# Kernel tuning notes

Hardware: AMD Instinct MI355X
Metric: run time of the kernel (lower is better)

## Reference

```python
import jax, jax.numpy as jnp
import numpy as np

EMBED_DIM = 1024
NUM_HEADS = 16
SCALE = (EMBED_DIM // NUM_HEADS) ** -0.5  # 0.125


def setup_inputs() -> dict:
    key = jax.random.key(0)
    ks = jax.random.split(key, 9)
    B, S, E = 4, 2048, EMBED_DIM
    std = E ** -0.5
    x = jax.random.normal(ks[0], (B, S, E), dtype=jnp.float32)
    Wq = jax.random.normal(ks[1], (E, E), dtype=jnp.float32) * std
    bq = jax.random.normal(ks[2], (E,), dtype=jnp.float32) * 0.01
    Wk = jax.random.normal(ks[3], (E, E), dtype=jnp.float32) * std
    bk = jax.random.normal(ks[4], (E,), dtype=jnp.float32) * 0.01
    Wv = jax.random.normal(ks[5], (E, E), dtype=jnp.float32) * std
    bv = jax.random.normal(ks[6], (E,), dtype=jnp.float32) * 0.01
    Wo = jax.random.normal(ks[7], (E, E), dtype=jnp.float32) * std
    bo = jax.random.normal(ks[8], (E,), dtype=jnp.float32) * 0.01
    return {"x": x, "Wq": Wq, "bq": bq, "Wk": Wk, "bk": bk,
            "Wv": Wv, "bv": bv, "Wo": Wo, "bo": bo}


def reference(x, Wq, bq, Wk, bk, Wv, bv, Wo, bo):
    # torch nn.Linear: y = x @ W.T + b
    q = jnp.einsum('bse,fe->bsf', x, Wq) + bq   # [B,S,E]
    k = jnp.einsum('bse,fe->bsf', x, Wk) + bk
    v = jnp.einsum('bse,fe->bsf', x, Wv) + bv
    # Bilinear (no softmax) attention: scores = (Q K^T) * scale
    scores = jnp.einsum('bse,bte->bst', q, k) * SCALE  # [B,S,S]
    out = jnp.einsum('bst,bte->bse', scores, v)        # [B,S,E]
    return jnp.einsum('bse,fe->bsf', out, Wo) + bo
```

## Files before the change

kernel.cpp:

```cpp
#include <hip/hip_runtime.h>
#include <stdint.h>

typedef __bf16 bf16_t;
typedef __bf16 bf16x8 __attribute__((ext_vector_type(8)));
typedef __bf16 bf16x4 __attribute__((ext_vector_type(4)));
typedef float floatx4 __attribute__((ext_vector_type(4)));

__device__ __forceinline__ void async_copy16(const bf16_t* g, bf16_t* l) {
  __builtin_amdgcn_global_load_lds(
      (const __attribute__((address_space(1))) void*)g,
      (__attribute__((address_space(3))) void*)l, 16, 0, 0);
}

struct CvtSeg { const float* s; bf16_t* d; long n; };
struct CvtArgs { CvtSeg seg[5]; };

__global__ void cvt_multi(CvtArgs a) {
  CvtSeg sg = a.seg[blockIdx.y];
  long i = ((long)blockIdx.x * blockDim.x + threadIdx.x) * 4;
  if (i < sg.n) {
    float4 f = *(const float4*)(sg.s + i);
    bf16x4 o;
    o[0] = (bf16_t)f.x; o[1] = (bf16_t)f.y; o[2] = (bf16_t)f.z; o[3] = (bf16_t)f.w;
    *(bf16x4*)(sg.d + i) = o;
  }
}

__global__ void reduce2_cvt(const float* __restrict__ a, const float* __restrict__ b,
                            bf16_t* __restrict__ d, long n) {
  long i = ((long)blockIdx.x * blockDim.x + threadIdx.x) * 4;
  if (i < n) {
    float4 x = *(const float4*)(a + i);
    float4 y = *(const float4*)(b + i);
    bf16x4 o;
    o[0] = (bf16_t)(x.x + y.x); o[1] = (bf16_t)(x.y + y.y);
    o[2] = (bf16_t)(x.z + y.z); o[3] = (bf16_t)(x.w + y.w);
    *(bf16x4*)(d + i) = o;
  }
}

__device__ __forceinline__ void gemm_core(
    const bf16_t* __restrict__ Ab, const bf16_t* __restrict__ Bb,
    int lda, int ldb, int nk, bf16_t* As, bf16_t* Bs,
    int m0, int n0, floatx4 (&acc)[4][4]) {
  const int tid  = threadIdx.x;
  const int lane = tid & 63;
  const int w    = tid >> 6;
  const int wr   = w >> 1, wc = w & 1;
  const int quad = lane >> 4, lm = lane & 15;
  const int ar = lane >> 2;
  const int ak = (((lane & 3) ^ ((ar >> 1) & 3))) * 8;
  const bf16_t* ag0 = Ab + (long)(m0 + w * 16 + ar) * lda + ak;
  const bf16_t* ag1 = ag0 + (long)64 * lda;
  const bf16_t* bg0 = Bb + (long)(n0 + w * 16 + ar) * ldb + ak;
  const bf16_t* bg1 = bg0 + (long)64 * ldb;
  const int swz = (lm >> 1) & 3;

  {
    bf16_t* la = As + w * 512;
    bf16_t* lb = Bs + w * 512;
    async_copy16(ag0, la);
    async_copy16(ag1, la + 2048);
    async_copy16(bg0, lb);
    async_copy16(bg1, lb + 2048);
  }
  for (int i = 0; i < nk; i++) {
    __syncthreads();
    if (i + 1 < nk) {
      const int buf = (i + 1) & 1;
      const int k0  = (i + 1) * 32;
      bf16_t* la = As + buf * 4096 + w * 512;
      bf16_t* lb = Bs + buf * 4096 + w * 512;
      async_copy16(ag0 + k0, la);
      async_copy16(ag1 + k0, la + 2048);
      async_copy16(bg0 + k0, lb);
      async_copy16(bg1 + k0, lb + 2048);
    }
    const bf16_t* Ar = As + (i & 1) * 4096;
    const bf16_t* Br = Bs + (i & 1) * 4096;
    bf16x8 afr[4], bfr[4];
#pragma unroll
    for (int r = 0; r < 4; r++)
      afr[r] = *(const bf16x8*)&Ar[(wr * 64 + r * 16 + lm) * 32 + (quad ^ swz) * 8];
#pragma unroll
    for (int c = 0; c < 4; c++)
      bfr[c] = *(const bf16x8*)&Br[(wc * 64 + c * 16 + lm) * 32 + (quad ^ swz) * 8];
#pragma unroll
    for (int r = 0; r < 4; r++)
#pragma unroll
      for (int c = 0; c < 4; c++)
        acc[r][c] = __builtin_amdgcn_mfma_f32_16x16x32_bf16(afr[r], bfr[c], acc[r][c], 0, 0, 0);
  }
}

__global__ __launch_bounds__(256, 2) void qkv3(
    const bf16_t* __restrict__ xb,
    const bf16_t* __restrict__ Wq, const bf16_t* __restrict__ Wk, const bf16_t* __restrict__ Wv,
    const float* __restrict__ bq, const float* __restrict__ bk, const float* __restrict__ bv,
    bf16_t* __restrict__ qout, bf16_t* __restrict__ kT, bf16_t* __restrict__ vT) {
  __shared__ bf16_t As[2 * 4096];
  __shared__ bf16_t Bsh[3][2 * 4096];
  const int L = blockIdx.x + (blockIdx.y << 3) + (blockIdx.z << 7);
  const int V = (L & 7) * 64 + (L >> 3);
  const int batch = V >> 7;
  const int rr_   = V & 127;
  const int n0 = (rr_ & 7) * 128;
  const int m0 = (rr_ >> 3) * 128;

  const int tid = threadIdx.x, lane = tid & 63, w = tid >> 6;
  const int wr = w >> 1, wc = w & 1, quad = lane >> 4, lm = lane & 15;
  const int ar = lane >> 2;
  const int ak = (((lane & 3) ^ ((ar >> 1) & 3))) * 8;
  const int swz = (lm >> 1) & 3;

  const bf16_t* ag0 = xb + (long)batch * (2048L * 1024) + (long)(m0 + w * 16 + ar) * 1024 + ak;
  const bf16_t* ag1 = ag0 + 64L * 1024;
  const bf16_t* Wp[3] = {Wq, Wk, Wv};
  const bf16_t* bg0[3];
  const bf16_t* bg1[3];
#pragma unroll
  for (int p = 0; p < 3; p++) {
    bg0[p] = Wp[p] + (long)(n0 + w * 16 + ar) * 1024 + ak;
    bg1[p] = bg0[p] + 64L * 1024;
  }

  floatx4 acc[3][4][4];
#pragma unroll
  for (int p = 0; p < 3; p++)
#pragma unroll
    for (int r = 0; r < 4; r++)
#pragma unroll
      for (int c = 0; c < 4; c++)
        acc[p][r][c] = (floatx4){0.f, 0.f, 0.f, 0.f};

  {
    bf16_t* la = As + w * 512;
    async_copy16(ag0, la);
    async_copy16(ag1, la + 2048);
#pragma unroll
    for (int p = 0; p < 3; p++) {
      bf16_t* lb = Bsh[p] + w * 512;
      async_copy16(bg0[p], lb);
      async_copy16(bg1[p], lb + 2048);
    }
  }
  for (int i = 0; i < 32; i++) {
    __syncthreads();
    if (i + 1 < 32) {
      const int buf = (i + 1) & 1, k0 = (i + 1) * 32;
      bf16_t* la = As + buf * 4096 + w * 512;
      async_copy16(ag0 + k0, la);
      async_copy16(ag1 + k0, la + 2048);
#pragma unroll
      for (int p = 0; p < 3; p++) {
        bf16_t* lb = Bsh[p] + buf * 4096 + w * 512;
        async_copy16(bg0[p] + k0, lb);
        async_copy16(bg1[p] + k0, lb + 2048);
      }
    }
    const bf16_t* Ar = As + (i & 1) * 4096;
    bf16x8 afr[4];
#pragma unroll
    for (int r = 0; r < 4; r++)
      afr[r] = *(const bf16x8*)&Ar[(wr * 64 + r * 16 + lm) * 32 + (quad ^ swz) * 8];
#pragma unroll
    for (int p = 0; p < 3; p++) {
      const bf16_t* Br = Bsh[p] + (i & 1) * 4096;
      bf16x8 bfr[4];
#pragma unroll
      for (int c = 0; c < 4; c++)
        bfr[c] = *(const bf16x8*)&Br[(wc * 64 + c * 16 + lm) * 32 + (quad ^ swz) * 8];
#pragma unroll
      for (int r = 0; r < 4; r++)
#pragma unroll
        for (int c = 0; c < 4; c++)
          acc[p][r][c] = __builtin_amdgcn_mfma_f32_16x16x32_bf16(afr[r], bfr[c], acc[p][r][c], 0, 0, 0);
    }
  }

  const int rowBase = m0 + wr * 64, colBase = n0 + wc * 64;
  {
    bf16_t* C = qout + (long)batch * (2048L * 1024);
#pragma unroll
    for (int r = 0; r < 4; r++) {
      const int row = rowBase + r * 16 + quad * 4;
#pragma unroll
      for (int c = 0; c < 4; c++) {
        const int col = colBase + c * 16 + lm;
        const float bv_ = bq[col];
#pragma unroll
        for (int i = 0; i < 4; i++)
          C[(long)(row + i) * 1024 + col] = (bf16_t)(acc[0][r][c][i] + bv_);
      }
    }
  }
#pragma unroll
  for (int p = 1; p < 3; p++) {
    bf16_t* C = ((p == 1) ? kT : vT) + (long)batch * (1024L * 2048);
    const float* bias = (p == 1) ? bk : bv;
#pragma unroll
    for (int r = 0; r < 4; r++) {
      const int row = rowBase + r * 16 + quad * 4;
#pragma unroll
      for (int c = 0; c < 4; c++) {
        const int col = colBase + c * 16 + lm;
        const float bv_ = bias[col];
        bf16x4 pk;
#pragma unroll
        for (int i = 0; i < 4; i++) pk[i] = (bf16_t)(acc[p][r][c][i] + bv_);
        *(bf16x4*)(C + (long)col * 2048 + row) = pk;
      }
    }
  }
}

template<int OUT_MODE, bool HAS_BIAS, int KSPLIT, int TOTAL, int BPZ, int GNX>
__global__ __launch_bounds__(256) void gemm_nt(
    const bf16_t* __restrict__ A, const bf16_t* __restrict__ B,
    void* __restrict__ C, void* __restrict__ C2, const float* __restrict__ bias,
    int lda, int ldb, int nk, long sA, long sB, long sC, int ldc, float alpha) {
  __shared__ bf16_t As[8192], Bs[8192];
  const int L = blockIdx.x + gridDim.x * (blockIdx.y + gridDim.y * blockIdx.z);
  const int V = (L & 7) * (TOTAL / 8) + (L >> 3);
  const int zp = V / BPZ;
  const int r_ = V % BPZ;
  const int n0 = (r_ % GNX) * 128;
  const int m0 = (r_ / GNX) * 128;
  const int nz = TOTAL / BPZ;
  const int nb = nz / KSPLIT;
  const int batch = zp % nb;
  const int kch   = zp / nb;
  const bf16_t* Ab = A + (long)batch * sA + (long)kch * (nk * 32);
  const bf16_t* Bb = B + (long)batch * sB + (long)kch * (nk * 32);

  floatx4 acc[4][4];
#pragma unroll
  for (int r = 0; r < 4; r++)
#pragma unroll
    for (int c = 0; c < 4; c++) acc[r][c] = (floatx4){0.f, 0.f, 0.f, 0.f};

  gemm_core(Ab, Bb, lda, ldb, nk, As, Bs, m0, n0, acc);

  const int lane = threadIdx.x & 63, w = threadIdx.x >> 6;
  const int wr = w >> 1, wc = w & 1, quad = lane >> 4, lm = lane & 15;
  const int rowBase = m0 + wr * 64, colBase = n0 + wc * 64;

  if (OUT_MODE == 0) {
    bf16_t* Cb = (bf16_t*)C + (long)batch * sC;
#pragma unroll
    for (int r = 0; r < 4; r++) {
      const int row = rowBase + r * 16 + quad * 4;
#pragma unroll
      for (int c = 0; c < 4; c++) {
        const int col = colBase + c * 16 + lm;
        const float bv_ = HAS_BIAS ? bias[col] : 0.f;
#pragma unroll
        for (int i = 0; i < 4; i++)
          Cb[(long)(row + i) * ldc + col] = (bf16_t)(acc[r][c][i] * alpha + bv_);
      }
    }
  } else if (OUT_MODE == 2) {
    float* Cf = (float*)C + (long)batch * sC;
#pragma unroll
    for (int r = 0; r < 4; r++) {
      const int row = rowBase + r * 16 + quad * 4;
#pragma unroll
      for (int c = 0; c < 4; c++) {
        const int col = colBase + c * 16 + lm;
        const float bv_ = HAS_BIAS ? bias[col] : 0.f;
#pragma unroll
        for (int i = 0; i < 4; i++)
          Cf[(long)(row + i) * ldc + col] = acc[r][c][i] * alpha + bv_;
      }
    }
  } else {
    float* Cf = (float*)(kch == 0 ? C : C2) + (long)batch * sC;
#pragma unroll
    for (int r = 0; r < 4; r++) {
      const int row = rowBase + r * 16 + quad * 4;
#pragma unroll
      for (int c = 0; c < 4; c++) {
        const int col = colBase + c * 16 + lm;
#pragma unroll
        for (int i = 0; i < 4; i++)
          Cf[(long)(row + i) * ldc + col] = acc[r][c][i] * alpha;
      }
    }
  }
}

extern "C" void kernel_launch(void* const* d_in, const int* in_sizes, int n_in,
                              void* d_out, int out_size, void* d_ws, size_t ws_size,
                              hipStream_t stream) {
  const float* x  = (const float*)d_in[0];
  const float* Wq = (const float*)d_in[1];
  const float* bq = (const float*)d_in[2];
  const float* Wk = (const float*)d_in[3];
  const float* bk = (const float*)d_in[4];
  const float* Wv = (const float*)d_in[5];
  const float* bv = (const float*)d_in[6];
  const float* Wo = (const float*)d_in[7];
  const float* bo = (const float*)d_in[8];
  float* out = (float*)d_out;

  const long NX = 8192L * 1024;
  const long NW = 1024L * 1024;
  const long NM = 4L * 1024 * 1024;

  bf16_t* ws  = (bf16_t*)d_ws;
  bf16_t* xb  = ws;
  bf16_t* Wqb = xb + NX;
  bf16_t* Wkb = Wqb + NW;
  bf16_t* Wvb = Wkb + NW;
  bf16_t* Wob = Wvb + NW;
  bf16_t* qb  = Wob + NW;
  bf16_t* kT  = qb + NX;
  bf16_t* vT  = kT + NX;
  float*  Mtf0 = (float*)xb;
  float*  Mtf1 = (float*)(vT + NX);
  bf16_t* MtTb = vT;
  bf16_t* Gb   = kT;

  CvtArgs ca;
  ca.seg[0] = {x,  xb,  NX};
  ca.seg[1] = {Wq, Wqb, NW};
  ca.seg[2] = {Wk, Wkb, NW};
  ca.seg[3] = {Wv, Wvb, NW};
  ca.seg[4] = {Wo, Wob, NW};
  cvt_multi<<<dim3(NX / 1024, 5), 256, 0, stream>>>(ca);

  qkv3<<<dim3(8, 16, 4), 256, 0, stream>>>(xb, Wqb, Wkb, Wvb, bq, bk, bv, qb, kT, vT);

  gemm_nt<3, false, 2, 512, 64, 8><<<dim3(8, 8, 8), 256, 0, stream>>>(
      kT, vT, Mtf0, Mtf1, nullptr, 2048, 2048, 32,
      1024L * 2048, 1024L * 2048, 1024L * 1024, 1024, 0.125f);

  reduce2_cvt<<<NM / 1024, 256, 0, stream>>>(Mtf0, Mtf1, MtTb, NM);

  gemm_nt<0, false, 1, 256, 64, 8><<<dim3(8, 8, 4), 256, 0, stream>>>(
      Wob, MtTb, Gb, nullptr, nullptr, 1024, 1024, 32,
      0L, 1024L * 1024, 1024L * 1024, 1024, 1.0f);

  gemm_nt<2, true, 1, 512, 128, 8><<<dim3(8, 16, 4), 256, 0, stream>>>(
      qb, Gb, out, nullptr, bo, 1024, 1024, 32,
      2048L * 1024, 1024L * 1024, 2048L * 1024, 1024, 1.0f);
}
```

Measured before the change: 243.7 us.

## Load QKV operands directly from global and drop split-K for KᵀV

The fused QKV projection kernel no longer stages tiles in LDS with async copies. Each wave now reads its MFMA fragments straight from global memory with 16-byte vector loads, and the launch bound no longer requests two blocks per CU. The KᵀV product stops splitting K into two fp32 partials plus a separate reduce-and-convert kernel; one pass over the full K writes bf16 directly. This removes a launch and the fp32 round trip, but the QKV kernel loses LDS reuse across waves, which risks much more global and L2 traffic, and the KᵀV grid halves.

```diff
diff --git a/kernel.cpp b/kernel.cpp
--- a/kernel.cpp
+++ b/kernel.cpp
@@ -23,19 +23,6 @@
     bf16x4 o;
     o[0] = (bf16_t)f.x; o[1] = (bf16_t)f.y; o[2] = (bf16_t)f.z; o[3] = (bf16_t)f.w;
     *(bf16x4*)(sg.d + i) = o;
-  }
-}
-
-__global__ void reduce2_cvt(const float* __restrict__ a, const float* __restrict__ b,
-                            bf16_t* __restrict__ d, long n) {
-  long i = ((long)blockIdx.x * blockDim.x + threadIdx.x) * 4;
-  if (i < n) {
-    float4 x = *(const float4*)(a + i);
-    float4 y = *(const float4*)(b + i);
-    bf16x4 o;
-    o[0] = (bf16_t)(x.x + y.x); o[1] = (bf16_t)(x.y + y.y);
-    o[2] = (bf16_t)(x.z + y.z); o[3] = (bf16_t)(x.w + y.w);
-    *(bf16x4*)(d + i) = o;
   }
 }
 
@@ -93,13 +80,11 @@
   }
 }
 
-__global__ __launch_bounds__(256, 2) void qkv3(
+__global__ __launch_bounds__(256) void qkv3(
     const bf16_t* __restrict__ xb,
     const bf16_t* __restrict__ Wq, const bf16_t* __restrict__ Wk, const bf16_t* __restrict__ Wv,
     const float* __restrict__ bq, const float* __restrict__ bk, const float* __restrict__ bv,
     bf16_t* __restrict__ qout, bf16_t* __restrict__ kT, bf16_t* __restrict__ vT) {
-  __shared__ bf16_t As[2 * 4096];
-  __shared__ bf16_t Bsh[3][2 * 4096];
   const int L = blockIdx.x + (blockIdx.y << 3) + (blockIdx.z << 7);
   const int V = (L & 7) * 64 + (L >> 3);
   const int batch = V >> 7;
@@ -109,20 +94,12 @@
 
   const int tid = threadIdx.x, lane = tid & 63, w = tid >> 6;
   const int wr = w >> 1, wc = w & 1, quad = lane >> 4, lm = lane & 15;
-  const int ar = lane >> 2;
-  const int ak = (((lane & 3) ^ ((ar >> 1) & 3))) * 8;
-  const int swz = (lm >> 1) & 3;
-
-  const bf16_t* ag0 = xb + (long)batch * (2048L * 1024) + (long)(m0 + w * 16 + ar) * 1024 + ak;
-  const bf16_t* ag1 = ag0 + 64L * 1024;
-  const bf16_t* Wp[3] = {Wq, Wk, Wv};
-  const bf16_t* bg0[3];
-  const bf16_t* bg1[3];
-#pragma unroll
-  for (int p = 0; p < 3; p++) {
-    bg0[p] = Wp[p] + (long)(n0 + w * 16 + ar) * 1024 + ak;
-    bg1[p] = bg0[p] + 64L * 1024;
-  }
+
+  const bf16_t* Abase = xb + (long)batch * (2048L * 1024)
+                      + (long)(m0 + wr * 64 + lm) * 1024 + quad * 8;
+  const bf16_t* Bq = Wq + (long)(n0 + wc * 64 + lm) * 1024 + quad * 8;
+  const bf16_t* Bk = Wk + (long)(n0 + wc * 64 + lm) * 1024 + quad * 8;
+  const bf16_t* Bv = Wv + (long)(n0 + wc * 64 + lm) * 1024 + quad * 8;
 
   floatx4 acc[3][4][4];
 #pragma unroll
@@ -133,48 +110,40 @@
       for (int c = 0; c < 4; c++)
         acc[p][r][c] = (floatx4){0.f, 0.f, 0.f, 0.f};
 
-  {
-    bf16_t* la = As + w * 512;
-    async_copy16(ag0, la);
-    async_copy16(ag1, la + 2048);
-#pragma unroll
-    for (int p = 0; p < 3; p++) {
-      bf16_t* lb = Bsh[p] + w * 512;
-      async_copy16(bg0[p], lb);
-      async_copy16(bg1[p], lb + 2048);
-    }
-  }
-  for (int i = 0; i < 32; i++) {
-    __syncthreads();
-    if (i + 1 < 32) {
-      const int buf = (i + 1) & 1, k0 = (i + 1) * 32;
-      bf16_t* la = As + buf * 4096 + w * 512;
-      async_copy16(ag0 + k0, la);
-      async_copy16(ag1 + k0, la + 2048);
-#pragma unroll
-      for (int p = 0; p < 3; p++) {
-        bf16_t* lb = Bsh[p] + buf * 4096 + w * 512;
-        async_copy16(bg0[p] + k0, lb);
-        async_copy16(bg1[p] + k0, lb + 2048);
-      }
-    }
-    const bf16_t* Ar = As + (i & 1) * 4096;
+  for (int k0 = 0; k0 < 1024; k0 += 32) {
     bf16x8 afr[4];
 #pragma unroll
     for (int r = 0; r < 4; r++)
-      afr[r] = *(const bf16x8*)&Ar[(wr * 64 + r * 16 + lm) * 32 + (quad ^ swz) * 8];
-#pragma unroll
-    for (int p = 0; p < 3; p++) {
-      const bf16_t* Br = Bsh[p] + (i & 1) * 4096;
+      afr[r] = *(const bf16x8*)(Abase + r * 16384 + k0);
+    {
       bf16x8 bfr[4];
 #pragma unroll
-      for (int c = 0; c < 4; c++)
-        bfr[c] = *(const bf16x8*)&Br[(wc * 64 + c * 16 + lm) * 32 + (quad ^ swz) * 8];
+      for (int c = 0; c < 4; c++) bfr[c] = *(const bf16x8*)(Bq + c * 16384 + k0);
 #pragma unroll
       for (int r = 0; r < 4; r++)
 #pragma unroll
         for (int c = 0; c < 4; c++)
-          acc[p][r][c] = __builtin_amdgcn_mfma_f32_16x16x32_bf16(afr[r], bfr[c], acc[p][r][c], 0, 0, 0);
+          acc[0][r][c] = __builtin_amdgcn_mfma_f32_16x16x32_bf16(afr[r], bfr[c], acc[0][r][c], 0, 0, 0);
+    }
+    {
+      bf16x8 bfr[4];
+#pragma unroll
+      for (int c = 0; c < 4; c++) bfr[c] = *(const bf16x8*)(Bk + c * 16384 + k0);
+#pragma unroll
+      for (int r = 0; r < 4; r++)
+#pragma unroll
+        for (int c = 0; c < 4; c++)
+          acc[1][r][c] = __builtin_amdgcn_mfma_f32_16x16x32_bf16(afr[r], bfr[c], acc[1][r][c], 0, 0, 0);
+    }
+    {
+      bf16x8 bfr[4];
+#pragma unroll
+      for (int c = 0; c < 4; c++) bfr[c] = *(const bf16x8*)(Bv + c * 16384 + k0);
+#pragma unroll
+      for (int r = 0; r < 4; r++)
+#pragma unroll
+        for (int c = 0; c < 4; c++)
+          acc[2][r][c] = __builtin_amdgcn_mfma_f32_16x16x32_bf16(afr[r], bfr[c], acc[2][r][c], 0, 0, 0);
     }
   }
 
@@ -214,24 +183,20 @@
   }
 }
 
-template<int OUT_MODE, bool HAS_BIAS, int KSPLIT, int TOTAL, int BPZ, int GNX>
+template<int OUT_MODE, bool HAS_BIAS, int TOTAL, int BPZ, int GNX>
 __global__ __launch_bounds__(256) void gemm_nt(
     const bf16_t* __restrict__ A, const bf16_t* __restrict__ B,
-    void* __restrict__ C, void* __restrict__ C2, const float* __restrict__ bias,
+    void* __restrict__ C, const float* __restrict__ bias,
     int lda, int ldb, int nk, long sA, long sB, long sC, int ldc, float alpha) {
   __shared__ bf16_t As[8192], Bs[8192];
   const int L = blockIdx.x + gridDim.x * (blockIdx.y + gridDim.y * blockIdx.z);
   const int V = (L & 7) * (TOTAL / 8) + (L >> 3);
-  const int zp = V / BPZ;
+  const int batch = V / BPZ;
   const int r_ = V % BPZ;
   const int n0 = (r_ % GNX) * 128;
   const int m0 = (r_ / GNX) * 128;
-  const int nz = TOTAL / BPZ;
-  const int nb = nz / KSPLIT;
-  const int batch = zp % nb;
-  const int kch   = zp / nb;
-  const bf16_t* Ab = A + (long)batch * sA + (long)kch * (nk * 32);
-  const bf16_t* Bb = B + (long)batch * sB + (long)kch * (nk * 32);
+  const bf16_t* Ab = A + (long)batch * sA;
+  const bf16_t* Bb = B + (long)batch * sB;
 
   floatx4 acc[4][4];
 #pragma unroll
@@ -259,7 +224,7 @@
           Cb[(long)(row + i) * ldc + col] = (bf16_t)(acc[r][c][i] * alpha + bv_);
       }
     }
-  } else if (OUT_MODE == 2) {
+  } else {
     float* Cf = (float*)C + (long)batch * sC;
 #pragma unroll
     for (int r = 0; r < 4; r++) {
@@ -271,19 +236,6 @@
 #pragma unroll
         for (int i = 0; i < 4; i++)
           Cf[(long)(row + i) * ldc + col] = acc[r][c][i] * alpha + bv_;
-      }
-    }
-  } else {
-    float* Cf = (float*)(kch == 0 ? C : C2) + (long)batch * sC;
-#pragma unroll
-    for (int r = 0; r < 4; r++) {
-      const int row = rowBase + r * 16 + quad * 4;
-#pragma unroll
-      for (int c = 0; c < 4; c++) {
-        const int col = colBase + c * 16 + lm;
-#pragma unroll
-        for (int i = 0; i < 4; i++)
-          Cf[(long)(row + i) * ldc + col] = acc[r][c][i] * alpha;
       }
     }
   }
@@ -316,10 +268,8 @@
   bf16_t* qb  = Wob + NW;
   bf16_t* kT  = qb + NX;
   bf16_t* vT  = kT + NX;
-  float*  Mtf0 = (float*)xb;
-  float*  Mtf1 = (float*)(vT + NX);
-  bf16_t* MtTb = vT;
-  bf16_t* Gb   = kT;
+  bf16_t* MtTb = vT + NX;
+  bf16_t* Gb   = xb;
 
   CvtArgs ca;
   ca.seg[0] = {x,  xb,  NX};
@@ -331,17 +281,15 @@
 
   qkv3<<<dim3(8, 16, 4), 256, 0, stream>>>(xb, Wqb, Wkb, Wvb, bq, bk, bv, qb, kT, vT);
 
-  gemm_nt<3, false, 2, 512, 64, 8><<<dim3(8, 8, 8), 256, 0, stream>>>(
-      kT, vT, Mtf0, Mtf1, nullptr, 2048, 2048, 32,
+  gemm_nt<0, false, 256, 64, 8><<<dim3(8, 8, 4), 256, 0, stream>>>(
+      kT, vT, MtTb, nullptr, 2048, 2048, 64,
       1024L * 2048, 1024L * 2048, 1024L * 1024, 1024, 0.125f);
 
-  reduce2_cvt<<<NM / 1024, 256, 0, stream>>>(Mtf0, Mtf1, MtTb, NM);
-
-  gemm_nt<0, false, 1, 256, 64, 8><<<dim3(8, 8, 4), 256, 0, stream>>>(
-      Wob, MtTb, Gb, nullptr, nullptr, 1024, 1024, 32,
+  gemm_nt<0, false, 256, 64, 8><<<dim3(8, 8, 4), 256, 0, stream>>>(
+      Wob, MtTb, Gb, nullptr, 1024, 1024, 32,
       0L, 1024L * 1024, 1024L * 1024, 1024, 1.0f);
 
-  gemm_nt<2, true, 1, 512, 128, 8><<<dim3(8, 16, 4), 256, 0, stream>>>(
-      qb, Gb, out, nullptr, bo, 1024, 1024, 32,
+  gemm_nt<2, true, 512, 128, 8><<<dim3(8, 16, 4), 256, 0, stream>>>(
+      qb, Gb, out, bo, 1024, 1024, 32,
       2048L * 1024, 1024L * 1024, 2048L * 1024, 1024, 1.0f);
 }
```

Measured after the change: 326.0 us. +33.8%, slower.
